# Performance work log

Hardware: AMD Instinct MI355X
Metric: run time of the kernel (lower is better)

## Reference

```python
import jax, jax.numpy as jnp
import numpy as np


def setup_inputs() -> dict:
    key = jax.random.key(0)
    x = jax.random.normal(key, (4, 3, 8192), dtype=jnp.float32)  # (B, 3, N)
    return {"x": x, "k": 30}


def reference(x, k):
    # x: (B, 3, N)
    x_t = jnp.swapaxes(x, 1, 2)  # (B, N, 3)
    xx = jnp.sum(x_t ** 2, axis=2, keepdims=True)  # (B, N, 1)
    # pairwise squared distances (B, N, N)
    pairwise = xx + jnp.swapaxes(xx, 1, 2) - 2.0 * jnp.matmul(x_t, x)
    # k smallest distances -> negate and take top_k
    _, idx = jax.lax.top_k(-pairwise, k)  # idx: (B, N, k)
    # gather neighbors: (B, N, k, 3)
    neighbors = jax.vmap(lambda pts, i: pts[i])(x_t, idx)
    centroid = jnp.mean(neighbors, axis=2, keepdims=True)  # (B, N, 1, 3)
    centered = neighbors - centroid  # (B, N, k, 3)
    # per-point 3x3 covariance
    cov = jnp.einsum('bnki,bnkj->bnij', centered, centered)  # (B, N, 3, 3)
    _, v = jnp.linalg.eigh(cov)  # eigenvalues ascending
    normals = v[..., :, 0]  # eigenvector of smallest eigenvalue, (B, N, 3)
    # orient normals toward viewpoint (origin): view_dir = -x_t
    dot = jnp.sum(-x_t * normals, axis=-1, keepdims=True)
    normals = jnp.where(dot < 0, -normals, normals)
    x_out = jnp.concatenate([x, jnp.swapaxes(normals, 1, 2)], axis=1)  # (B, 6, N)
    return x_out
```

## Files before the change

kernel.cpp:

```cpp
#include <hip/hip_runtime.h>
#include <math.h>

#define N_PTS   8192
#define KNN     30
#define CAPG    104
#define STR     105
#define GROUPS  8
#define BLOCK   128
#define NZ      64
#define NY      64
#define NBKT    (NZ * NY)
#define CLO     -4.0f
#define CSC     8.0f
#define INVCSC  0.125f
#define LAMBDA  40.0
#define RBINS   2048
#define RWMAX   32.0f
#define RSCALE  ((float)RBINS / RWMAX)


__device__ __forceinline__ int clampi(int v, int lo, int hi) {
    return v < lo ? lo : (v > hi ? hi : v);
}
__device__ __forceinline__ int bucket_of(float pz, float py) {
    int zb = clampi((int)floorf((pz - CLO) * CSC), 0, NZ - 1);
    int yb = clampi((int)floorf((py - CLO) * CSC), 0, NY - 1);
    return (zb << 6) | yb;
}

__global__ __launch_bounds__(1024) void prep_kernel(const float* __restrict__ x,
                                                    float4* __restrict__ S,
                                                    int* __restrict__ O,
                                                    int* __restrict__ bstart,
                                                    float* __restrict__ out) {
    __shared__ int hist[NBKT];
    __shared__ int cur[NBKT];
    __shared__ int wsum[16];

    const int b = blockIdx.x;
    const int t = threadIdx.x;
    const int wid = t >> 6, lane = t & 63;
    const float* xb = x + (size_t)b * 3 * N_PTS;
    float* ob = out + (size_t)b * 6 * N_PTS;

    for (int k = t; k < NBKT; k += 1024) hist[k] = 0;
    __syncthreads();

    float px[8], py[8], pz[8];
    int   bk[8];
    #pragma unroll
    for (int u = 0; u < 8; ++u) {
        int i = (u << 10) + t;
        px[u] = xb[i]; py[u] = xb[N_PTS + i]; pz[u] = xb[2 * N_PTS + i];
        bk[u] = bucket_of(pz[u], py[u]);
        atomicAdd(&hist[bk[u]], 1);
        ob[i]             = px[u];
        ob[N_PTS + i]     = py[u];
        ob[2 * N_PTS + i] = pz[u];
    }
    __syncthreads();

    int l0 = hist[4 * t], l1 = hist[4 * t + 1], l2 = hist[4 * t + 2], l3 = hist[4 * t + 3];
    int s = l0 + l1 + l2 + l3;
    int sum = s;
    #pragma unroll
    for (int off = 1; off < 64; off <<= 1) {
        int v = __shfl_up(sum, off);
        if (lane >= off) sum += v;
    }
    if (lane == 63) wsum[wid] = sum;
    __syncthreads();
    if (t == 0) {
        int run = 0;
        #pragma unroll
        for (int k = 0; k < 16; ++k) { int v = wsum[k]; wsum[k] = run; run += v; }
    }
    __syncthreads();
    int base = wsum[wid] + (sum - s);
    int b0 = base, b1 = base + l0, b2 = b1 + l1, b3 = b2 + l2;
    cur[4 * t] = b0; cur[4 * t + 1] = b1; cur[4 * t + 2] = b2; cur[4 * t + 3] = b3;
    int* bsb = bstart + b * (NBKT + 1);
    bsb[4 * t] = b0; bsb[4 * t + 1] = b1; bsb[4 * t + 2] = b2; bsb[4 * t + 3] = b3;
    if (t == 1023) bsb[NBKT] = N_PTS;
    __syncthreads();

    float4* Sb = S + ((size_t)b << 13);
    int*    Ob = O + ((size_t)b << 13);
    #pragma unroll
    for (int u = 0; u < 8; ++u) {
        int dst = atomicAdd(&cur[bk[u]], 1);
        float xx = __fadd_rn(__fadd_rn(__fmul_rn(px[u], px[u]), __fmul_rn(py[u], py[u])),
                             __fmul_rn(pz[u], pz[u]));
        Sb[dst] = make_float4(px[u], py[u], pz[u], xx);
        Ob[dst] = (u << 10) + t;
    }
}

__global__ __launch_bounds__(BLOCK, 6) void knn_normal_kernel(const float4* __restrict__ S,
                                                              const int* __restrict__ O,
                                                              const int* __restrict__ bstart,
                                                              const float* __restrict__ R2T,
                                                              float* __restrict__ out) {
    __shared__ unsigned long long ldk[GROUPS * STR];

    const int t    = threadIdx.x;
    const int l16  = t & 15;
    const int g    = t >> 4;
    const int gsh  = (t & 63) & ~15;
    const int qblk = (blockIdx.x * 1031) & 4095;
    const int qid  = qblk * GROUPS + g;
    const int b    = qid >> 13;
    const int pos  = qid & (N_PTS - 1);
    const float4* __restrict__ P  = S + ((size_t)b << 13);
    const int*    __restrict__ Ob = O + ((size_t)b << 13);
    const int*    __restrict__ bs = bstart + b * (NBKT + 1);
    const float4 qp = P[pos];
    const int    oi = Ob[pos];

    unsigned long long* __restrict__ ldg = ldk + g * STR;

    const int rbin = min((int)(qp.w * RSCALE), RBINS - 1);
    float r2 = R2T[rbin];

    int  cnt = 0;
    bool active = true;

    for (;;) {
        if (active) {
            cnt = 0;
            float w  = __fmaf_rn(sqrtf(r2), 1.002f, 1e-3f);
            float w2 = __fmul_rn(w, w);
            int zlo = clampi((int)floorf((qp.z - w - CLO) * CSC), 0, NZ - 1);
            int zhi = clampi((int)floorf((qp.z + w - CLO) * CSC), 0, NZ - 1);
            for (int zb = zlo; zb <= zhi; ++zb) {
                float z0  = CLO + (float)zb * INVCSC;
                float dzr = fmaxf(fmaxf(z0 - qp.z, qp.z - (z0 + INVCSC)), 0.0f) * 0.999f;
                float hw2 = __fmaf_rn(-dzr, dzr, w2);
                if (hw2 <= 0.0f) continue;
                float hw  = __fmaf_rn(sqrtf(hw2), 1.001f, 1e-4f);
                int ylo = clampi((int)floorf((qp.y - hw - CLO) * CSC), 0, NY - 1);
                int yhi = clampi((int)floorf((qp.y + hw - CLO) * CSC), 0, NY - 1);
                int lo = bs[(zb << 6) + ylo];
                int hi = bs[(zb << 6) + yhi + 1];
                int smax = (hi - lo + 31) >> 5;
                for (int s = 0; s < smax; ++s) {
                    int j1  = lo + (s << 5) + l16;
                    int j2  = j1 + 16;
                    int jc1 = j1 < hi ? j1 : hi - 1;
                    int jc2 = j2 < hi ? j2 : hi - 1;
                    float4 p1 = P[jc1];
                    float4 p2 = P[jc2];
                    float mm1 = __fmaf_rn(qp.z, p1.z, __fmaf_rn(qp.y, p1.y, __fmul_rn(qp.x, p1.x)));
                    float d1  = __fsub_rn(__fadd_rn(qp.w, p1.w), __fmul_rn(2.0f, mm1));
                    float mm2 = __fmaf_rn(qp.z, p2.z, __fmaf_rn(qp.y, p2.y, __fmul_rn(qp.x, p2.x)));
                    float d2  = __fsub_rn(__fadd_rn(qp.w, p2.w), __fmul_rn(2.0f, mm2));
                    bool hit1 = (j1 < hi) && (d1 <= r2);
                    bool hit2 = (j2 < hi) && (d2 <= r2);
                    unsigned long long m1 = __ballot(hit1);
                    unsigned sub1 = (unsigned)((m1 >> gsh) & 0xFFFFull);
                    if (hit1) {
                        int slot = cnt + __popc(sub1 & ((1u << l16) - 1u));
                        if (slot < CAPG) {
                            unsigned u = __float_as_uint(d1);
                            u = (u & 0x80000000u) ? ~u : (u | 0x80000000u);
                            ldg[slot] = ((unsigned long long)u << 28) | (unsigned long long)jc1;
                        }
                    }
                    cnt += __popc(sub1);
                    unsigned long long m2 = __ballot(hit2);
                    unsigned sub2 = (unsigned)((m2 >> gsh) & 0xFFFFull);
                    if (hit2) {
                        int slot = cnt + __popc(sub2 & ((1u << l16) - 1u));
                        if (slot < CAPG) {
                            unsigned u = __float_as_uint(d2);
                            u = (u & 0x80000000u) ? ~u : (u | 0x80000000u);
                            ldg[slot] = ((unsigned long long)u << 28) | (unsigned long long)jc2;
                        }
                    }
                    cnt += __popc(sub2);
                }
            }
        }
        bool bad = active && (cnt < KNN || cnt > CAPG);
        if (__ballot(bad) == 0ULL) break;
        active = bad;
        if (active) r2 = (cnt < KNN) ? r2 * 1.6f : r2 * 0.82f;
    }

    for (int k = l16; k < cnt; k += 16) {
        unsigned long long key = ldg[k];
        int jc = (int)(key & 0x3FFFull);
        ldg[k] = (key & ~0x0FFFFFFFull) | ((unsigned long long)Ob[jc] << 14) | (unsigned long long)jc;
    }
    __syncthreads();

    const double qx = (double)qp.x, qy = (double)qp.y, qz = (double)qp.z;
    double sx = 0.0, sy = 0.0, sz = 0.0;
    double sxx = 0.0, sxy = 0.0, sxz = 0.0, syy = 0.0, syz = 0.0, szz = 0.0;

    for (int k = l16; k < cnt; k += 16) {
        unsigned long long key = ldg[k];
        int rank = 0;
        for (int u = 0; u < cnt; ++u) rank += (ldg[u] < key) ? 1 : 0;
        if (rank < KNN) {
            float4 p = P[(int)(key & 0x3FFFull)];
            double ax = (double)p.x - qx, ay = (double)p.y - qy, az = (double)p.z - qz;
            sx += ax; sy += ay; sz += az;
            sxx = fma(ax, ax, sxx); sxy = fma(ax, ay, sxy); sxz = fma(ax, az, sxz);
            syy = fma(ay, ay, syy); syz = fma(ay, az, syz); szz = fma(az, az, szz);
        }
    }

    #pragma unroll
    for (int off = 1; off < 16; off <<= 1) {
        sx  += __shfl_xor(sx,  off, 16); sy  += __shfl_xor(sy,  off, 16); sz  += __shfl_xor(sz,  off, 16);
        sxx += __shfl_xor(sxx, off, 16); sxy += __shfl_xor(sxy, off, 16); sxz += __shfl_xor(sxz, off, 16);
        syy += __shfl_xor(syy, off, 16); syz += __shfl_xor(syz, off, 16); szz += __shfl_xor(szz, off, 16);
    }

    if (l16 == 0) {
        const double kinv = 1.0 / (double)KNN;
        double m00 = sxx - sx * sx * kinv;
        double m11 = syy - sy * sy * kinv;
        double m22 = szz - sz * sz * kinv;
        double m01 = sxy - sx * sy * kinv;
        double m02 = sxz - sx * sz * kinv;
        double m12 = syz - sy * sz * kinv;

        double nx = 1.0, ny = 0.0, nz = 0.0;
        double q3 = (m00 + m11 + m22) / 3.0;
        double p1 = m01 * m01 + m02 * m02 + m12 * m12;
        double d00 = m00 - q3, d11 = m11 - q3, d22 = m22 - q3;
        double p2 = d00 * d00 + d11 * d11 + d22 * d22 + 2.0 * p1;
        if (p2 > 1e-280) {
            double pp = sqrt(p2 / 6.0);
            double ip = 1.0 / pp;
            double b00 = d00 * ip, b11 = d11 * ip, b22 = d22 * ip;
            double b01 = m01 * ip, b02 = m02 * ip, b12 = m12 * ip;
            double detB = b00 * (b11 * b22 - b12 * b12)
                        - b01 * (b01 * b22 - b12 * b02)
                        + b02 * (b01 * b12 - b11 * b02);
            double rr = 0.5 * detB;
            rr = rr < -1.0 ? -1.0 : (rr > 1.0 ? 1.0 : rr);
            double phi = acos(rr) / 3.0;
            double lam = q3 + 2.0 * pp * cos(phi + 2.0943951023931953);
            double a00 = m00 - lam, a11 = m11 - lam, a22 = m22 - lam;
            double v0x = m01 * m12 - m02 * a11, v0y = m02 * m01 - a00 * m12, v0z = a00 * a11 - m01 * m01;
            double v1x = m01 * a22 - m02 * m12, v1y = m02 * m02 - a00 * a22, v1z = a00 * m12 - m01 * m02;
            double v2x = a11 * a22 - m12 * m12, v2y = m12 * m02 - m01 * a22, v2z = m01 * m12 - a11 * m02;
            double n0 = v0x * v0x + v0y * v0y + v0z * v0z;
            double n1 = v1x * v1x + v1y * v1y + v1z * v1z;
            double n2 = v2x * v2x + v2y * v2y + v2z * v2z;
            double bx = v0x, by = v0y, bz = v0z, bn = n0;
            if (n1 > bn) { bx = v1x; by = v1y; bz = v1z; bn = n1; }
            if (n2 > bn) { bx = v2x; by = v2y; bz = v2z; bn = n2; }
            if (bn > 1e-280) {
                double inv = 1.0 / sqrt(bn);
                nx = bx * inv; ny = by * inv; nz = bz * inv;
            }
        }
        double dq = -(qx * nx + qy * ny + qz * nz);
        if (dq < 0.0) { nx = -nx; ny = -ny; nz = -nz; }

        float* ob = out + (size_t)b * 6 * N_PTS;
        ob[3 * N_PTS + oi] = (float)nx;
        ob[4 * N_PTS + oi] = (float)ny;
        ob[5 * N_PTS + oi] = (float)nz;
    }
}

static float  g_r2t[RBINS];
static bool   g_r2t_init = false;

static void build_r2t_host() {
    for (int k = 0; k < RBINS; ++k) {
        double wrep = ((double)k + 0.5) * ((double)RWMAX / (double)RBINS);
        double c = sqrt(wrep); if (c < 1e-3) c = 1e-3;
        double rlo = 0.05, rhi = 6.0;
        for (int it = 0; it < 40; ++it) {
            double r = 0.5 * (rlo + rhi);
            double slo = c - r; if (slo < 0.0) slo = 0.0;
            double h = (c + r - slo) * 0.125;
            double f = 0.0;
            for (int l = 0; l <= 8; ++l) {
                double sq = slo + h * (double)l;
                double cs = c - sq;
                double hh = (r * r - cs * cs) * (0.5 / c);
                double cap = 2.0 * sq;
                if (hh > cap) hh = cap;
                if (hh < 0.0) hh = 0.0;
                double wq = (l == 0 || l == 8) ? 1.0 : ((l & 1) ? 4.0 : 2.0);
                f += wq * exp(-0.5 * sq * sq) * sq * hh;
            }
            double lam = 1089.3 * f * h;
            if (lam < (double)LAMBDA) rlo = r; else rhi = r;
        }
        double rad = rhi * 1.02;
        g_r2t[k] = (float)(rad * rad);
    }
}

extern "C" void kernel_launch(void* const* d_in, const int* in_sizes, int n_in,
                              void* d_out, int out_size, void* d_ws, size_t ws_size,
                              hipStream_t stream) {
    const float* x = (const float*)d_in[0];
    float* out = (float*)d_out;
    char* ws = (char*)d_ws;
    float4* S    = (float4*)(ws);
    int*    O    = (int*)(ws + 524288);
    int*    bsta = (int*)(ws + 655360);
    float*  r2t  = (float*)(ws + 720912);

    if (!g_r2t_init) { build_r2t_host(); g_r2t_init = true; }
    hipMemcpyAsync(r2t, g_r2t, RBINS * sizeof(float), hipMemcpyHostToDevice, stream);

    prep_kernel<<<dim3(4), dim3(1024), 0, stream>>>(x, S, O, bsta, out);
    knn_normal_kernel<<<dim3(32768 / GROUPS), dim3(BLOCK), 0, stream>>>(S, O, bsta, r2t, out);
}
```

Baseline: 156.4 us.

## Cooperatively scan heavy KNN queries with whole wavefront, regroup queries by batch

Result: no change. 156.6 us (+0.1%).

```diff
diff --git a/kernel.cpp b/kernel.cpp
--- a/kernel.cpp
+++ b/kernel.cpp
@@ -7,6 +7,7 @@
 #define STR     105
 #define GROUPS  8
 #define BLOCK   128
+#define NBLK    4096
 #define NZ      64
 #define NY      64
 #define NBKT    (NZ * NY)
@@ -17,6 +18,7 @@
 #define RBINS   2048
 #define RWMAX   32.0f
 #define RSCALE  ((float)RBINS / RWMAX)
+#define THRESH  1024
 
 
 __device__ __forceinline__ int clampi(int v, int lo, int hi) {
@@ -104,34 +106,119 @@
     __shared__ unsigned long long ldk[GROUPS * STR];
 
     const int t    = threadIdx.x;
+    const int lane = t & 63;
     const int l16  = t & 15;
-    const int g    = t >> 4;
-    const int gsh  = (t & 63) & ~15;
-    const int qblk = (blockIdx.x * 1031) & 4095;
-    const int qid  = qblk * GROUPS + g;
-    const int b    = qid >> 13;
-    const int pos  = qid & (N_PTS - 1);
+    const int wv   = t >> 6;
+    const int gw   = (t >> 4) & 3;
+    const int gsh  = lane & ~15;
+    const int w    = (blockIdx.x << 1) | wv;
+    const int wpos = (w * 2531) & (N_PTS - 1);
+    const int qid  = (gw << 13) | wpos;
+    const int b    = gw;
+    const int pos  = wpos;
     const float4* __restrict__ P  = S + ((size_t)b << 13);
     const int*    __restrict__ Ob = O + ((size_t)b << 13);
     const int*    __restrict__ bs = bstart + b * (NBKT + 1);
     const float4 qp = P[pos];
     const int    oi = Ob[pos];
 
-    unsigned long long* __restrict__ ldg = ldk + g * STR;
-
-    const int rbin = min((int)(qp.w * RSCALE), RBINS - 1);
-    float r2 = R2T[rbin];
-
-    int  cnt = 0;
-    bool active = true;
+    unsigned long long* __restrict__ ldg = ldk + ((wv << 2) + gw) * STR;
+
+    float r2 = R2T[min((int)(qp.w * RSCALE), RBINS - 1)];
+    int tot;
+    {
+        float ww = __fmaf_rn(sqrtf(r2), 1.002f, 1e-3f);
+        int zlo = clampi((int)floorf((qp.z - ww - CLO) * CSC), 0, NZ - 1);
+        int zhi = clampi((int)floorf((qp.z + ww - CLO) * CSC), 0, NZ - 1);
+        int ylo = clampi((int)floorf((qp.y - ww - CLO) * CSC), 0, NY - 1);
+        int yhi = clampi((int)floorf((qp.y + ww - CLO) * CSC), 0, NY - 1);
+        int tsum = 0;
+        for (int zb = zlo + l16; zb <= zhi; zb += 16)
+            tsum += bs[(zb << 6) + yhi + 1] - bs[(zb << 6) + ylo];
+        tsum += __shfl_xor(tsum, 1, 16); tsum += __shfl_xor(tsum, 2, 16);
+        tsum += __shfl_xor(tsum, 4, 16); tsum += __shfl_xor(tsum, 8, 16);
+        tot = tsum;
+    }
+    const bool heavy = tot > THRESH;
+    const unsigned long long hm = __ballot(heavy);
+
+    int mycnt = 0;
+    for (int h = 0; h < 4; ++h) {
+        if (!((hm >> (h << 4)) & 1ull)) continue;
+        const float4* __restrict__ Ph  = S + ((size_t)h << 13);
+        const int*    __restrict__ bsh = bstart + h * (NBKT + 1);
+        const float4 qh = Ph[wpos];
+        float r2h = R2T[min((int)(qh.w * RSCALE), RBINS - 1)];
+        unsigned long long* __restrict__ row = ldk + ((wv << 2) + h) * STR;
+        int cnth;
+        for (;;) {
+            cnth = 0;
+            float ww  = __fmaf_rn(sqrtf(r2h), 1.002f, 1e-3f);
+            float w2  = __fmul_rn(ww, ww);
+            int zlo = clampi((int)floorf((qh.z - ww - CLO) * CSC), 0, NZ - 1);
+            int zhi = clampi((int)floorf((qh.z + ww - CLO) * CSC), 0, NZ - 1);
+            for (int zb = zlo; zb <= zhi; ++zb) {
+                float z0  = CLO + (float)zb * INVCSC;
+                float dzr = fmaxf(fmaxf(z0 - qh.z, qh.z - (z0 + INVCSC)), 0.0f) * 0.999f;
+                float hw2 = __fmaf_rn(-dzr, dzr, w2);
+                if (hw2 <= 0.0f) continue;
+                float hw  = __fmaf_rn(sqrtf(hw2), 1.001f, 1e-4f);
+                int ylo = clampi((int)floorf((qh.y - hw - CLO) * CSC), 0, NY - 1);
+                int yhi = clampi((int)floorf((qh.y + hw - CLO) * CSC), 0, NY - 1);
+                int lo = bsh[(zb << 6) + ylo];
+                int hi = bsh[(zb << 6) + yhi + 1];
+                int smax = (hi - lo + 127) >> 7;
+                for (int s = 0; s < smax; ++s) {
+                    int j1  = lo + (s << 7) + lane;
+                    int j2  = j1 + 64;
+                    int jc1 = j1 < hi ? j1 : hi - 1;
+                    int jc2 = j2 < hi ? j2 : hi - 1;
+                    float4 p1 = Ph[jc1];
+                    float4 p2 = Ph[jc2];
+                    float mm1 = __fmaf_rn(qh.z, p1.z, __fmaf_rn(qh.y, p1.y, __fmul_rn(qh.x, p1.x)));
+                    float d1  = __fsub_rn(__fadd_rn(qh.w, p1.w), __fmul_rn(2.0f, mm1));
+                    float mm2 = __fmaf_rn(qh.z, p2.z, __fmaf_rn(qh.y, p2.y, __fmul_rn(qh.x, p2.x)));
+                    float d2  = __fsub_rn(__fadd_rn(qh.w, p2.w), __fmul_rn(2.0f, mm2));
+                    bool hit1 = (j1 < hi) && (d1 <= r2h);
+                    bool hit2 = (j2 < hi) && (d2 <= r2h);
+                    unsigned long long m1 = __ballot(hit1);
+                    if (hit1) {
+                        int slot = cnth + __popcll(m1 & ((1ull << lane) - 1ull));
+                        if (slot < CAPG) {
+                            unsigned u = __float_as_uint(d1);
+                            u = (u & 0x80000000u) ? ~u : (u | 0x80000000u);
+                            row[slot] = ((unsigned long long)u << 28) | (unsigned long long)jc1;
+                        }
+                    }
+                    cnth += __popcll(m1);
+                    unsigned long long m2 = __ballot(hit2);
+                    if (hit2) {
+                        int slot = cnth + __popcll(m2 & ((1ull << lane) - 1ull));
+                        if (slot < CAPG) {
+                            unsigned u = __float_as_uint(d2);
+                            u = (u & 0x80000000u) ? ~u : (u | 0x80000000u);
+                            row[slot] = ((unsigned long long)u << 28) | (unsigned long long)jc2;
+                        }
+                    }
+                    cnth += __popcll(m2);
+                }
+            }
+            if (cnth >= KNN && cnth <= CAPG) break;
+            r2h = (cnth < KNN) ? r2h * 1.6f : r2h * 0.82f;
+        }
+        if (gw == h) mycnt = cnth;
+    }
+
+    int  cnt = mycnt;
+    bool active = !heavy;
 
     for (;;) {
         if (active) {
             cnt = 0;
-            float w  = __fmaf_rn(sqrtf(r2), 1.002f, 1e-3f);
-            float w2 = __fmul_rn(w, w);
-            int zlo = clampi((int)floorf((qp.z - w - CLO) * CSC), 0, NZ - 1);
-            int zhi = clampi((int)floorf((qp.z + w - CLO) * CSC), 0, NZ - 1);
+            float ww = __fmaf_rn(sqrtf(r2), 1.002f, 1e-3f);
+            float w2 = __fmul_rn(ww, ww);
+            int zlo = clampi((int)floorf((qp.z - ww - CLO) * CSC), 0, NZ - 1);
+            int zhi = clampi((int)floorf((qp.z + ww - CLO) * CSC), 0, NZ - 1);
             for (int zb = zlo; zb <= zhi; ++zb) {
                 float z0  = CLO + (float)zb * INVCSC;
                 float dzr = fmaxf(fmaxf(z0 - qp.z, qp.z - (z0 + INVCSC)), 0.0f) * 0.999f;
@@ -187,12 +274,16 @@
         if (active) r2 = (cnt < KNN) ? r2 * 1.6f : r2 * 0.82f;
     }
 
+    __builtin_amdgcn_wave_barrier();
+    asm volatile("s_waitcnt lgkmcnt(0)" ::: "memory");
+
     for (int k = l16; k < cnt; k += 16) {
         unsigned long long key = ldg[k];
         int jc = (int)(key & 0x3FFFull);
         ldg[k] = (key & ~0x0FFFFFFFull) | ((unsigned long long)Ob[jc] << 14) | (unsigned long long)jc;
     }
-    __syncthreads();
+    __builtin_amdgcn_wave_barrier();
+    asm volatile("s_waitcnt lgkmcnt(0)" ::: "memory");
 
     const double qx = (double)qp.x, qy = (double)qp.y, qz = (double)qp.z;
     double sx = 0.0, sy = 0.0, sz = 0.0;
@@ -315,5 +406,5 @@
     hipMemcpyAsync(r2t, g_r2t, RBINS * sizeof(float), hipMemcpyHostToDevice, stream);
 
     prep_kernel<<<dim3(4), dim3(1024), 0, stream>>>(x, S, O, bsta, out);
-    knn_normal_kernel<<<dim3(32768 / GROUPS), dim3(BLOCK), 0, stream>>>(S, O, bsta, r2t, out);
-}
+    knn_normal_kernel<<<dim3(NBLK), dim3(BLOCK), 0, stream>>>(S, O, bsta, r2t, out);
+}
```
